# Optimization experiments

Measured on AMD Instinct MI355X. Metric: run time of the kernel, lower is better.

The kernel has to match this reference:

```python
import jax, jax.numpy as jnp
from jax import lax
import numpy as np

INPUT_SIZE = 1
HIDDEN = 32
NUM_LAYERS = 2
OUTPUT_SIZE = 1
FC1 = 16
B, T = 4096, 512


def _lstm_layer(x, w_ih, w_hh, b_ih, b_hh):
    """One LSTM layer, batch_first x: [B,T,in] -> outputs [B,T,H], (h_T, c_T).
    PyTorch gate order: i, f, g, o."""
    Bsz = x.shape[0]
    H = w_hh.shape[1]
    # Precompute input projections for all timesteps: [B,T,4H]
    xp = jnp.einsum('bti,gi->btg', x, w_ih) + b_ih + b_hh
    xp_t = jnp.swapaxes(xp, 0, 1)  # [T,B,4H]

    def step(carry, xt):
        h, c = carry
        gates = xt + h @ w_hh.T  # [B,4H]
        i, f, g, o = jnp.split(gates, 4, axis=-1)
        i = jax.nn.sigmoid(i)
        f = jax.nn.sigmoid(f)
        g = jnp.tanh(g)
        o = jax.nn.sigmoid(o)
        c = f * c + i * g
        h = o * jnp.tanh(c)
        return (h, c), h

    h0 = jnp.zeros((Bsz, H), dtype=x.dtype)
    c0 = jnp.zeros((Bsz, H), dtype=x.dtype)
    (hT, cT), hs = lax.scan(step, (h0, c0), xp_t)
    return jnp.swapaxes(hs, 0, 1), (hT, cT)


def setup_inputs() -> dict:
    key = jax.random.key(0)
    ks = jax.random.split(key, 12)
    s = 1.0 / np.sqrt(HIDDEN)

    def u(k, shape):
        return jax.random.uniform(k, shape, jnp.float32, -s, s)

    x = jax.random.normal(ks[0], (B, T, INPUT_SIZE), jnp.float32)
    return {
        'x': x,
        'w_ih0': u(ks[1], (4 * HIDDEN, INPUT_SIZE)),
        'w_hh0': u(ks[2], (4 * HIDDEN, HIDDEN)),
        'b_ih0': u(ks[3], (4 * HIDDEN,)),
        'b_hh0': u(ks[4], (4 * HIDDEN,)),
        'w_ih1': u(ks[5], (4 * HIDDEN, HIDDEN)),
        'w_hh1': u(ks[6], (4 * HIDDEN, HIDDEN)),
        'b_ih1': u(ks[7], (4 * HIDDEN,)),
        'b_hh1': u(ks[8], (4 * HIDDEN,)),
        'fc1_w': u(ks[9], (FC1, HIDDEN)),
        'fc1_b': jnp.zeros((FC1,), jnp.float32),
        'fc2_w': u(ks[10], (OUTPUT_SIZE, FC1)),
        'fc2_b': jnp.zeros((OUTPUT_SIZE,), jnp.float32),
    }


def reference(x, w_ih0, w_hh0, b_ih0, b_hh0, w_ih1, w_hh1, b_ih1, b_hh1,
              fc1_w, fc1_b, fc2_w, fc2_b):
    # Layer 0: need full output sequence to feed layer 1.
    h_seq, _ = _lstm_layer(x, w_ih0, w_hh0, b_ih0, b_hh0)
    # (inter-layer dropout is identity at inference)
    # Layer 1: only final hidden state is used downstream.
    _, (hT, _) = _lstm_layer(h_seq, w_ih1, w_hh1, b_ih1, b_hh1)
    # Head (dropouts identity at inference): fc1 -> relu -> fc2
    out = jax.nn.relu(hT @ fc1_w.T + fc1_b)
    out = out @ fc2_w.T + fc2_b  # [B, output_size]
    return out
```

## Files before the change

kernel.cpp:

```cpp
#include <hip/hip_runtime.h>

#define TLEN 512
#define XSTR 516
#define HSTR 40

typedef __attribute__((ext_vector_type(8))) short bf16x8;
typedef __attribute__((ext_vector_type(4))) float f32x4;

#define LOG2E_ 1.44269504f

__device__ __forceinline__ float fexp2_(float x) {
#if __has_builtin(__builtin_amdgcn_exp2f)
    return __builtin_amdgcn_exp2f(x);
#else
    return __expf(x * 0.69314718056f);
#endif
}
__device__ __forceinline__ float frcp_(float x) {
#if __has_builtin(__builtin_amdgcn_rcpf)
    return __builtin_amdgcn_rcpf(x);
#else
    return 1.0f / x;
#endif
}
__device__ __forceinline__ float sigmoidf_(float x) {
    return frcp_(1.0f + fexp2_(-LOG2E_ * x));
}
__device__ __forceinline__ float tanhf_(float x) {
    return 1.0f - 2.0f * frcp_(1.0f + fexp2_((2.0f * LOG2E_) * x));
}
__device__ __forceinline__ unsigned short f2bf(float f) {
    unsigned u = __float_as_uint(f);
    u += 0x7FFFu + ((u >> 16) & 1u);
    return (unsigned short)(u >> 16);
}
__device__ __forceinline__ float bf2f(unsigned short b) {
    return __uint_as_float(((unsigned)b) << 16);
}

__global__ __launch_bounds__(512, 1)
void lstm2_mfma(const float* __restrict__ x,
                const float* __restrict__ w_ih0,
                const float* __restrict__ w_hh0,
                const float* __restrict__ b_ih0,
                const float* __restrict__ b_hh0,
                const float* __restrict__ w_ih1,
                const float* __restrict__ w_hh1,
                const float* __restrict__ b_ih1,
                const float* __restrict__ b_hh1,
                const float* __restrict__ fc1_w,
                const float* __restrict__ fc1_b,
                const float* __restrict__ fc2_w,
                const float* __restrict__ fc2_b,
                float* __restrict__ out)
{
    __shared__ float x_lds[16][XSTR];
    __shared__ unsigned short h0b[2][2][16][HSTR];
    __shared__ unsigned short h1b[2][2][16][HSTR];
    __shared__ float h1f[16][36];

    const int tid  = threadIdx.x;
    const int wid  = tid >> 6;
    const int lane = tid & 63;
    const int col  = lane & 15;
    const int kq   = lane >> 4;
    const int b0   = blockIdx.x * 16;

    for (int i4 = tid; i4 < (16 * TLEN) / 4; i4 += 512) {
        const int idx = i4 * 4;
        const int row = idx >> 9, cx = idx & 511;
        float4 v = *(const float4*)(x + (long)(b0 + row) * TLEN + cx);
        *(float4*)&x_lds[row][cx] = v;
    }
    for (int i = tid; i < 2 * 2 * 16 * HSTR; i += 512) {
        ((unsigned short*)h0b)[i] = 0;
        ((unsigned short*)h1b)[i] = 0;
    }

    const bool L0    = (wid < 4);
    const int  w4    = wid & 3;
    const int  tile0 = 2 * w4;
    const int  tile1 = 2 * w4 + 1;
    const int  j0    = 4 * tile0 + kq;
    const int  j1    = 4 * tile1 + kq;
    const int  k0    = kq * 8;

    const int arow0 = (col & 3) * 32 + 4 * tile0 + (col >> 2);
    const int arow1 = (col & 3) * 32 + 4 * tile1 + (col >> 2);

    const float* WA = L0 ? w_hh0 : w_ih1;
    bf16x8 wA0hi, wA0lo, wA1hi, wA1lo;
    bf16x8 wB0hi, wB0lo, wB1hi, wB1lo;
    #pragma unroll
    for (int e = 0; e < 8; ++e) {
        float w;
        unsigned short hb;
        w = WA[arow0 * 32 + k0 + e]; hb = f2bf(w);
        wA0hi[e] = (short)hb; wA0lo[e] = (short)f2bf(w - bf2f(hb));
        w = WA[arow1 * 32 + k0 + e]; hb = f2bf(w);
        wA1hi[e] = (short)hb; wA1lo[e] = (short)f2bf(w - bf2f(hb));
        w = L0 ? 0.0f : w_hh1[arow0 * 32 + k0 + e]; hb = f2bf(w);
        wB0hi[e] = (short)hb; wB0lo[e] = (short)f2bf(w - bf2f(hb));
        w = L0 ? 0.0f : w_hh1[arow1 * 32 + k0 + e]; hb = f2bf(w);
        wB1hi[e] = (short)hb; wB1lo[e] = (short)f2bf(w - bf2f(hb));
    }

    f32x4 bias0, bias1, xw0v, xw1v;
    #pragma unroll
    for (int r = 0; r < 4; ++r) {
        const int r0 = r * 32 + 4 * tile0 + kq;
        const int r1 = r * 32 + 4 * tile1 + kq;
        bias0[r] = L0 ? (b_ih0[r0] + b_hh0[r0]) : (b_ih1[r0] + b_hh1[r0]);
        bias1[r] = L0 ? (b_ih0[r1] + b_hh0[r1]) : (b_ih1[r1] + b_hh1[r1]);
        xw0v[r]  = L0 ? w_ih0[r0] : 0.0f;
        xw1v[r]  = L0 ? w_ih0[r1] : 0.0f;
    }

    float c0_ = 0.0f, c1_ = 0.0f;
    __syncthreads();

#define STEP_BODY(T, CUR, PRV)                                                   \
    do {                                                                         \
        const int t_ = (T);                                                      \
        if (L0) {                                                                \
            if (t_ < TLEN) {                                                     \
                const bf16x8 bhi = *(const bf16x8*)&h0b[PRV][0][col][k0];        \
                const bf16x8 blo = *(const bf16x8*)&h0b[PRV][1][col][k0];        \
                const float  xt  = x_lds[col][t_];                               \
                f32x4 a0 = bias0 + xw0v * xt;                                    \
                f32x4 a1 = bias1 + xw1v * xt;                                    \
                a0 = __builtin_amdgcn_mfma_f32_16x16x32_bf16(wA0hi, bhi, a0, 0, 0, 0); \
                a1 = __builtin_amdgcn_mfma_f32_16x16x32_bf16(wA1hi, bhi, a1, 0, 0, 0); \
                a0 = __builtin_amdgcn_mfma_f32_16x16x32_bf16(wA0hi, blo, a0, 0, 0, 0); \
                a1 = __builtin_amdgcn_mfma_f32_16x16x32_bf16(wA1hi, blo, a1, 0, 0, 0); \
                a0 = __builtin_amdgcn_mfma_f32_16x16x32_bf16(wA0lo, bhi, a0, 0, 0, 0); \
                a1 = __builtin_amdgcn_mfma_f32_16x16x32_bf16(wA1lo, bhi, a1, 0, 0, 0); \
                {                                                                \
                    const float iv = sigmoidf_(a0[0]), fv = sigmoidf_(a0[1]);    \
                    const float gv = tanhf_(a0[2]),    ov = sigmoidf_(a0[3]);    \
                    c0_ = fv * c0_ + iv * gv;                                    \
                    const float hv = ov * tanhf_(c0_);                           \
                    const unsigned u = __float_as_uint(hv);                      \
                    h0b[CUR][0][col][j0] = (unsigned short)(u >> 16);            \
                    const float lof = hv - __uint_as_float(u & 0xFFFF0000u);     \
                    h0b[CUR][1][col][j0] = (unsigned short)(__float_as_uint(lof) >> 16); \
                }                                                                \
                {                                                                \
                    const float iv = sigmoidf_(a1[0]), fv = sigmoidf_(a1[1]);    \
                    const float gv = tanhf_(a1[2]),    ov = sigmoidf_(a1[3]);    \
                    c1_ = fv * c1_ + iv * gv;                                    \
                    const float hv = ov * tanhf_(c1_);                           \
                    const unsigned u = __float_as_uint(hv);                      \
                    h0b[CUR][0][col][j1] = (unsigned short)(u >> 16);            \
                    const float lof = hv - __uint_as_float(u & 0xFFFF0000u);     \
                    h0b[CUR][1][col][j1] = (unsigned short)(__float_as_uint(lof) >> 16); \
                }                                                                \
            }                                                                    \
        } else {                                                                 \
            if (t_ >= 1) {                                                       \
                const bf16x8 a0hi = *(const bf16x8*)&h0b[PRV][0][col][k0];       \
                const bf16x8 a0lo = *(const bf16x8*)&h0b[PRV][1][col][k0];       \
                const bf16x8 a1hi = *(const bf16x8*)&h1b[CUR][0][col][k0];       \
                const bf16x8 a1lo = *(const bf16x8*)&h1b[CUR][1][col][k0];       \
                f32x4 a0 = bias0;                                                \
                f32x4 a1 = bias1;                                                \
                a0 = __builtin_amdgcn_mfma_f32_16x16x32_bf16(wA0hi, a0hi, a0, 0, 0, 0); \
                a1 = __builtin_amdgcn_mfma_f32_16x16x32_bf16(wA1hi, a0hi, a1, 0, 0, 0); \
                a0 = __builtin_amdgcn_mfma_f32_16x16x32_bf16(wA0hi, a0lo, a0, 0, 0, 0); \
                a1 = __builtin_amdgcn_mfma_f32_16x16x32_bf16(wA1hi, a0lo, a1, 0, 0, 0); \
                a0 = __builtin_amdgcn_mfma_f32_16x16x32_bf16(wA0lo, a0hi, a0, 0, 0, 0); \
                a1 = __builtin_amdgcn_mfma_f32_16x16x32_bf16(wA1lo, a0hi, a1, 0, 0, 0); \
                a0 = __builtin_amdgcn_mfma_f32_16x16x32_bf16(wB0hi, a1hi, a0, 0, 0, 0); \
                a1 = __builtin_amdgcn_mfma_f32_16x16x32_bf16(wB1hi, a1hi, a1, 0, 0, 0); \
                a0 = __builtin_amdgcn_mfma_f32_16x16x32_bf16(wB0hi, a1lo, a0, 0, 0, 0); \
                a1 = __builtin_amdgcn_mfma_f32_16x16x32_bf16(wB1hi, a1lo, a1, 0, 0, 0); \
                a0 = __builtin_amdgcn_mfma_f32_16x16x32_bf16(wB0lo, a1hi, a0, 0, 0, 0); \
                a1 = __builtin_amdgcn_mfma_f32_16x16x32_bf16(wB1lo, a1hi, a1, 0, 0, 0); \
                float hv0f, hv1f;                                                \
                {                                                                \
                    const float iv = sigmoidf_(a0[0]), fv = sigmoidf_(a0[1]);    \
                    const float gv = tanhf_(a0[2]),    ov = sigmoidf_(a0[3]);    \
                    c0_ = fv * c0_ + iv * gv;                                    \
                    const float hv = ov * tanhf_(c0_);                           \
                    hv0f = hv;                                                   \
                    const unsigned u = __float_as_uint(hv);                      \
                    h1b[PRV][0][col][j0] = (unsigned short)(u >> 16);            \
                    const float lof = hv - __uint_as_float(u & 0xFFFF0000u);     \
                    h1b[PRV][1][col][j0] = (unsigned short)(__float_as_uint(lof) >> 16); \
                }                                                                \
                {                                                                \
                    const float iv = sigmoidf_(a1[0]), fv = sigmoidf_(a1[1]);    \
                    const float gv = tanhf_(a1[2]),    ov = sigmoidf_(a1[3]);    \
                    c1_ = fv * c1_ + iv * gv;                                    \
                    const float hv = ov * tanhf_(c1_);                           \
                    hv1f = hv;                                                   \
                    const unsigned u = __float_as_uint(hv);                      \
                    h1b[PRV][0][col][j1] = (unsigned short)(u >> 16);            \
                    const float lof = hv - __uint_as_float(u & 0xFFFF0000u);     \
                    h1b[PRV][1][col][j1] = (unsigned short)(__float_as_uint(lof) >> 16); \
                }                                                                \
                if (t_ == TLEN) { h1f[col][j0] = hv0f; h1f[col][j1] = hv1f; }    \
            }                                                                    \
        }                                                                        \
        __syncthreads();                                                         \
    } while (0)

    STEP_BODY(0, 0, 1);
    for (int tt = 1; tt < TLEN; tt += 2) {
        STEP_BODY(tt,     1, 0);
        STEP_BODY(tt + 1, 0, 1);
    }
#undef STEP_BODY

    if (wid == 0) {
        float s = 0.0f;
        #pragma unroll
        for (int it = 0; it < 4; ++it) {
            const int r = kq * 4 + it;
            float acc = fc1_b[r];
            #pragma unroll
            for (int qq = 0; qq < 8; ++qq) {
                const float4 wv = *(const float4*)(fc1_w + r * 32 + qq * 4);
                const float4 hv = *(const float4*)&h1f[col][qq * 4];
                acc += wv.x * hv.x + wv.y * hv.y + wv.z * hv.z + wv.w * hv.w;
            }
            s += fmaxf(acc, 0.0f) * fc2_w[r];
        }
        s += __shfl_xor(s, 16);
        s += __shfl_xor(s, 32);
        if (lane < 16) out[b0 + col] = s + fc2_b[0];
    }
}

extern "C" void kernel_launch(void* const* d_in, const int* in_sizes, int n_in,
                              void* d_out, int out_size, void* d_ws, size_t ws_size,
                              hipStream_t stream) {
    const float* x     = (const float*)d_in[0];
    const float* w_ih0 = (const float*)d_in[1];
    const float* w_hh0 = (const float*)d_in[2];
    const float* b_ih0 = (const float*)d_in[3];
    const float* b_hh0 = (const float*)d_in[4];
    const float* w_ih1 = (const float*)d_in[5];
    const float* w_hh1 = (const float*)d_in[6];
    const float* b_ih1 = (const float*)d_in[7];
    const float* b_hh1 = (const float*)d_in[8];
    const float* fc1_w = (const float*)d_in[9];
    const float* fc1_b = (const float*)d_in[10];
    const float* fc2_w = (const float*)d_in[11];
    const float* fc2_b = (const float*)d_in[12];
    float* out = (float*)d_out;

    dim3 grid(4096 / 16);
    dim3 block(512);
    hipLaunchKernelGGL(lstm2_mfma, grid, block, 0, stream,
                       x, w_ih0, w_hh0, b_ih0, b_hh0,
                       w_ih1, w_hh1, b_ih1, b_hh1,
                       fc1_w, fc1_b, fc2_w, fc2_b, out);
}
```

Before: 247.1 us.

## Give every wave one tile of both LSTM layers and fold activation scales into weights

Instead of splitting the block into four layer-0 waves and four layer-1 waves that each handle two gate tiles, every one of the eight waves now computes one tile for layer 0 and one tile for layer 1 in each step. This balances the uneven MFMA work between the layers (3 vs 6 MFMAs per tile) across all waves. It also pre-multiplies weights and biases by -log2e, or by 2*log2e for the g gate, so the sigmoid and tanh evaluations drop their input multiplies. The cost is more weight registers per wave and scaling applied before the bf16 hi/lo split, which slightly changes rounding.

```diff
diff --git a/kernel.cpp b/kernel.cpp
--- a/kernel.cpp
+++ b/kernel.cpp
@@ -8,6 +8,7 @@
 typedef __attribute__((ext_vector_type(4))) float f32x4;
 
 #define LOG2E_ 1.44269504f
+#define S2F_   2.88539008f
 
 __device__ __forceinline__ float fexp2_(float x) {
 #if __has_builtin(__builtin_amdgcn_exp2f)
@@ -23,12 +24,6 @@
     return 1.0f / x;
 #endif
 }
-__device__ __forceinline__ float sigmoidf_(float x) {
-    return frcp_(1.0f + fexp2_(-LOG2E_ * x));
-}
-__device__ __forceinline__ float tanhf_(float x) {
-    return 1.0f - 2.0f * frcp_(1.0f + fexp2_((2.0f * LOG2E_) * x));
-}
 __device__ __forceinline__ unsigned short f2bf(float f) {
     unsigned u = __float_as_uint(f);
     u += 0x7FFFu + ((u >> 16) & 1u);
@@ -36,6 +31,17 @@
 }
 __device__ __forceinline__ float bf2f(unsigned short b) {
     return __uint_as_float(((unsigned)b) << 16);
+}
+
+__device__ __forceinline__ float lstm_nl(const f32x4 a, float& cS) {
+    const float i_ = frcp_(1.0f + fexp2_(a[0]));
+    const float f_ = frcp_(1.0f + fexp2_(a[1]));
+    const float rg = frcp_(1.0f + fexp2_(a[2]));
+    const float g_ = S2F_ - 2.0f * S2F_ * rg;
+    const float o_ = frcp_(1.0f + fexp2_(a[3]));
+    cS = f_ * cS + i_ * g_;
+    const float rc = frcp_(1.0f + fexp2_(cS));
+    return o_ * (1.0f - 2.0f * rc);
 }
 
 __global__ __launch_bounds__(512, 1)
@@ -77,130 +83,74 @@
         ((unsigned short*)h1b)[i] = 0;
     }
 
-    const bool L0    = (wid < 4);
-    const int  w4    = wid & 3;
-    const int  tile0 = 2 * w4;
-    const int  tile1 = 2 * w4 + 1;
-    const int  j0    = 4 * tile0 + kq;
-    const int  j1    = 4 * tile1 + kq;
-    const int  k0    = kq * 8;
-
-    const int arow0 = (col & 3) * 32 + 4 * tile0 + (col >> 2);
-    const int arow1 = (col & 3) * 32 + 4 * tile1 + (col >> 2);
-
-    const float* WA = L0 ? w_hh0 : w_ih1;
-    bf16x8 wA0hi, wA0lo, wA1hi, wA1lo;
-    bf16x8 wB0hi, wB0lo, wB1hi, wB1lo;
+    const int tile = wid;
+    const int jj   = 4 * tile + kq;
+    const int k0   = kq * 8;
+
+    const int   arow = (col & 3) * 32 + 4 * tile + (col >> 2);
+    const float sA   = ((col & 3) == 2) ? S2F_ : -LOG2E_;
+
+    bf16x8 wL0hi, wL0lo, wIhi, wIlo, wHhi, wHlo;
     #pragma unroll
     for (int e = 0; e < 8; ++e) {
         float w;
         unsigned short hb;
-        w = WA[arow0 * 32 + k0 + e]; hb = f2bf(w);
-        wA0hi[e] = (short)hb; wA0lo[e] = (short)f2bf(w - bf2f(hb));
-        w = WA[arow1 * 32 + k0 + e]; hb = f2bf(w);
-        wA1hi[e] = (short)hb; wA1lo[e] = (short)f2bf(w - bf2f(hb));
-        w = L0 ? 0.0f : w_hh1[arow0 * 32 + k0 + e]; hb = f2bf(w);
-        wB0hi[e] = (short)hb; wB0lo[e] = (short)f2bf(w - bf2f(hb));
-        w = L0 ? 0.0f : w_hh1[arow1 * 32 + k0 + e]; hb = f2bf(w);
-        wB1hi[e] = (short)hb; wB1lo[e] = (short)f2bf(w - bf2f(hb));
-    }
-
-    f32x4 bias0, bias1, xw0v, xw1v;
+        w = sA * w_hh0[arow * 32 + k0 + e]; hb = f2bf(w);
+        wL0hi[e] = (short)hb; wL0lo[e] = (short)f2bf(w - bf2f(hb));
+        w = sA * w_ih1[arow * 32 + k0 + e]; hb = f2bf(w);
+        wIhi[e]  = (short)hb; wIlo[e]  = (short)f2bf(w - bf2f(hb));
+        w = sA * w_hh1[arow * 32 + k0 + e]; hb = f2bf(w);
+        wHhi[e]  = (short)hb; wHlo[e]  = (short)f2bf(w - bf2f(hb));
+    }
+
+    f32x4 biasL0, biasL1, xwv;
     #pragma unroll
     for (int r = 0; r < 4; ++r) {
-        const int r0 = r * 32 + 4 * tile0 + kq;
-        const int r1 = r * 32 + 4 * tile1 + kq;
-        bias0[r] = L0 ? (b_ih0[r0] + b_hh0[r0]) : (b_ih1[r0] + b_hh1[r0]);
-        bias1[r] = L0 ? (b_ih0[r1] + b_hh0[r1]) : (b_ih1[r1] + b_hh1[r1]);
-        xw0v[r]  = L0 ? w_ih0[r0] : 0.0f;
-        xw1v[r]  = L0 ? w_ih0[r1] : 0.0f;
-    }
-
-    float c0_ = 0.0f, c1_ = 0.0f;
+        const int  row = r * 32 + 4 * tile + kq;
+        const float sr = (r == 2) ? S2F_ : -LOG2E_;
+        biasL0[r] = sr * (b_ih0[row] + b_hh0[row]);
+        biasL1[r] = sr * (b_ih1[row] + b_hh1[row]);
+        xwv[r]    = sr * w_ih0[row];
+    }
+
+    float cL0 = 0.0f, cL1 = 0.0f;
     __syncthreads();
+
+#define PACK_H(BUF, PAR, HV, J)                                                  \
+    do {                                                                         \
+        const unsigned u_ = __float_as_uint(HV);                                 \
+        BUF[PAR][0][col][J] = (unsigned short)(u_ >> 16);                        \
+        const float lof_ = (HV) - __uint_as_float(u_ & 0xFFFF0000u);             \
+        BUF[PAR][1][col][J] = (unsigned short)(__float_as_uint(lof_) >> 16);     \
+    } while (0)
 
 #define STEP_BODY(T, CUR, PRV)                                                   \
     do {                                                                         \
         const int t_ = (T);                                                      \
-        if (L0) {                                                                \
-            if (t_ < TLEN) {                                                     \
-                const bf16x8 bhi = *(const bf16x8*)&h0b[PRV][0][col][k0];        \
-                const bf16x8 blo = *(const bf16x8*)&h0b[PRV][1][col][k0];        \
-                const float  xt  = x_lds[col][t_];                               \
-                f32x4 a0 = bias0 + xw0v * xt;                                    \
-                f32x4 a1 = bias1 + xw1v * xt;                                    \
-                a0 = __builtin_amdgcn_mfma_f32_16x16x32_bf16(wA0hi, bhi, a0, 0, 0, 0); \
-                a1 = __builtin_amdgcn_mfma_f32_16x16x32_bf16(wA1hi, bhi, a1, 0, 0, 0); \
-                a0 = __builtin_amdgcn_mfma_f32_16x16x32_bf16(wA0hi, blo, a0, 0, 0, 0); \
-                a1 = __builtin_amdgcn_mfma_f32_16x16x32_bf16(wA1hi, blo, a1, 0, 0, 0); \
-                a0 = __builtin_amdgcn_mfma_f32_16x16x32_bf16(wA0lo, bhi, a0, 0, 0, 0); \
-                a1 = __builtin_amdgcn_mfma_f32_16x16x32_bf16(wA1lo, bhi, a1, 0, 0, 0); \
-                {                                                                \
-                    const float iv = sigmoidf_(a0[0]), fv = sigmoidf_(a0[1]);    \
-                    const float gv = tanhf_(a0[2]),    ov = sigmoidf_(a0[3]);    \
-                    c0_ = fv * c0_ + iv * gv;                                    \
-                    const float hv = ov * tanhf_(c0_);                           \
-                    const unsigned u = __float_as_uint(hv);                      \
-                    h0b[CUR][0][col][j0] = (unsigned short)(u >> 16);            \
-                    const float lof = hv - __uint_as_float(u & 0xFFFF0000u);     \
-                    h0b[CUR][1][col][j0] = (unsigned short)(__float_as_uint(lof) >> 16); \
-                }                                                                \
-                {                                                                \
-                    const float iv = sigmoidf_(a1[0]), fv = sigmoidf_(a1[1]);    \
-                    const float gv = tanhf_(a1[2]),    ov = sigmoidf_(a1[3]);    \
-                    c1_ = fv * c1_ + iv * gv;                                    \
-                    const float hv = ov * tanhf_(c1_);                           \
-                    const unsigned u = __float_as_uint(hv);                      \
-                    h0b[CUR][0][col][j1] = (unsigned short)(u >> 16);            \
-                    const float lof = hv - __uint_as_float(u & 0xFFFF0000u);     \
-                    h0b[CUR][1][col][j1] = (unsigned short)(__float_as_uint(lof) >> 16); \
-                }                                                                \
-            }                                                                    \
-        } else {                                                                 \
-            if (t_ >= 1) {                                                       \
-                const bf16x8 a0hi = *(const bf16x8*)&h0b[PRV][0][col][k0];       \
-                const bf16x8 a0lo = *(const bf16x8*)&h0b[PRV][1][col][k0];       \
-                const bf16x8 a1hi = *(const bf16x8*)&h1b[CUR][0][col][k0];       \
-                const bf16x8 a1lo = *(const bf16x8*)&h1b[CUR][1][col][k0];       \
-                f32x4 a0 = bias0;                                                \
-                f32x4 a1 = bias1;                                                \
-                a0 = __builtin_amdgcn_mfma_f32_16x16x32_bf16(wA0hi, a0hi, a0, 0, 0, 0); \
-                a1 = __builtin_amdgcn_mfma_f32_16x16x32_bf16(wA1hi, a0hi, a1, 0, 0, 0); \
-                a0 = __builtin_amdgcn_mfma_f32_16x16x32_bf16(wA0hi, a0lo, a0, 0, 0, 0); \
-                a1 = __builtin_amdgcn_mfma_f32_16x16x32_bf16(wA1hi, a0lo, a1, 0, 0, 0); \
-                a0 = __builtin_amdgcn_mfma_f32_16x16x32_bf16(wA0lo, a0hi, a0, 0, 0, 0); \
-                a1 = __builtin_amdgcn_mfma_f32_16x16x32_bf16(wA1lo, a0hi, a1, 0, 0, 0); \
-                a0 = __builtin_amdgcn_mfma_f32_16x16x32_bf16(wB0hi, a1hi, a0, 0, 0, 0); \
-                a1 = __builtin_amdgcn_mfma_f32_16x16x32_bf16(wB1hi, a1hi, a1, 0, 0, 0); \
-                a0 = __builtin_amdgcn_mfma_f32_16x16x32_bf16(wB0hi, a1lo, a0, 0, 0, 0); \
-                a1 = __builtin_amdgcn_mfma_f32_16x16x32_bf16(wB1hi, a1lo, a1, 0, 0, 0); \
-                a0 = __builtin_amdgcn_mfma_f32_16x16x32_bf16(wB0lo, a1hi, a0, 0, 0, 0); \
-                a1 = __builtin_amdgcn_mfma_f32_16x16x32_bf16(wB1lo, a1hi, a1, 0, 0, 0); \
-                float hv0f, hv1f;                                                \
-                {                                                                \
-                    const float iv = sigmoidf_(a0[0]), fv = sigmoidf_(a0[1]);    \
-                    const float gv = tanhf_(a0[2]),    ov = sigmoidf_(a0[3]);    \
-                    c0_ = fv * c0_ + iv * gv;                                    \
-                    const float hv = ov * tanhf_(c0_);                           \
-                    hv0f = hv;                                                   \
-                    const unsigned u = __float_as_uint(hv);                      \
-                    h1b[PRV][0][col][j0] = (unsigned short)(u >> 16);            \
-                    const float lof = hv - __uint_as_float(u & 0xFFFF0000u);     \
-                    h1b[PRV][1][col][j0] = (unsigned short)(__float_as_uint(lof) >> 16); \
-                }                                                                \
-                {                                                                \
-                    const float iv = sigmoidf_(a1[0]), fv = sigmoidf_(a1[1]);    \
-                    const float gv = tanhf_(a1[2]),    ov = sigmoidf_(a1[3]);    \
-                    c1_ = fv * c1_ + iv * gv;                                    \
-                    const float hv = ov * tanhf_(c1_);                           \
-                    hv1f = hv;                                                   \
-                    const unsigned u = __float_as_uint(hv);                      \
-                    h1b[PRV][0][col][j1] = (unsigned short)(u >> 16);            \
-                    const float lof = hv - __uint_as_float(u & 0xFFFF0000u);     \
-                    h1b[PRV][1][col][j1] = (unsigned short)(__float_as_uint(lof) >> 16); \
-                }                                                                \
-                if (t_ == TLEN) { h1f[col][j0] = hv0f; h1f[col][j1] = hv1f; }    \
-            }                                                                    \
+        const bf16x8 bhi = *(const bf16x8*)&h0b[PRV][0][col][k0];                \
+        const bf16x8 blo = *(const bf16x8*)&h0b[PRV][1][col][k0];                \
+        if (t_ < TLEN) {                                                         \
+            const float xt = x_lds[col][t_];                                     \
+            f32x4 aL0 = biasL0 + xwv * xt;                                       \
+            aL0 = __builtin_amdgcn_mfma_f32_16x16x32_bf16(wL0hi, bhi, aL0, 0, 0, 0); \
+            aL0 = __builtin_amdgcn_mfma_f32_16x16x32_bf16(wL0hi, blo, aL0, 0, 0, 0); \
+            aL0 = __builtin_amdgcn_mfma_f32_16x16x32_bf16(wL0lo, bhi, aL0, 0, 0, 0); \
+            const float hv = lstm_nl(aL0, cL0);                                  \
+            PACK_H(h0b, CUR, hv, jj);                                            \
+        }                                                                        \
+        if (t_ >= 1) {                                                           \
+            const bf16x8 chi = *(const bf16x8*)&h1b[CUR][0][col][k0];            \
+            const bf16x8 clo = *(const bf16x8*)&h1b[CUR][1][col][k0];            \
+            f32x4 aL1 = biasL1;                                                  \
+            aL1 = __builtin_amdgcn_mfma_f32_16x16x32_bf16(wIhi, bhi, aL1, 0, 0, 0); \
+            aL1 = __builtin_amdgcn_mfma_f32_16x16x32_bf16(wIhi, blo, aL1, 0, 0, 0); \
+            aL1 = __builtin_amdgcn_mfma_f32_16x16x32_bf16(wIlo, bhi, aL1, 0, 0, 0); \
+            aL1 = __builtin_amdgcn_mfma_f32_16x16x32_bf16(wHhi, chi, aL1, 0, 0, 0); \
+            aL1 = __builtin_amdgcn_mfma_f32_16x16x32_bf16(wHhi, clo, aL1, 0, 0, 0); \
+            aL1 = __builtin_amdgcn_mfma_f32_16x16x32_bf16(wHlo, chi, aL1, 0, 0, 0); \
+            const float hv = lstm_nl(aL1, cL1);                                  \
+            PACK_H(h1b, PRV, hv, jj);                                            \
+            if (t_ == TLEN) h1f[col][jj] = hv;                                   \
         }                                                                        \
         __syncthreads();                                                         \
     } while (0)
@@ -211,6 +161,7 @@
         STEP_BODY(tt + 1, 0, 1);
     }
 #undef STEP_BODY
+#undef PACK_H
 
     if (wid == 0) {
         float s = 0.0f;
```

New measurement: 235.5 us. 1.05x faster.
